# Optimization experiments

Hardware: AMD Instinct MI355X
Metric: run time of the kernel (lower is better)

Reference implementation:

```python
import jax, jax.numpy as jnp
import numpy as np

B, L, D = 4, 4096, 1024


def hippo_freqs(dim):
    n = np.arange(dim, dtype=np.float32)
    f = np.sqrt(2 * n + 1)
    f = f / f.max()
    return np.exp(-f * np.log(10000)).astype(np.float32)


def setup_inputs() -> dict:
    key = jax.random.key(0)
    ks = jax.random.split(key, 8)
    s = 1.0 / np.sqrt(D)
    return {
        "x": jax.random.normal(ks[0], (B, L, D), dtype=jnp.float32),
        "omega": jnp.asarray(hippo_freqs(D)),
        "log_gamma": jax.random.normal(ks[1], (D,), dtype=jnp.float32) - 3.0,
        "dt": jnp.float32(0.1),
        "W_psi": jax.random.uniform(ks[2], (2 * D, D), jnp.float32, -s, s),
        "b_psi": jax.random.uniform(ks[3], (2 * D,), jnp.float32, -s, s),
        "W_phi": jax.random.uniform(ks[4], (2 * D, D), jnp.float32, -s, s),
        "b_phi": jax.random.uniform(ks[5], (2 * D,), jnp.float32, -s, s),
        "W_gate": jax.random.uniform(ks[6], (D, D), jnp.float32, -s, s),
        "b_gate": jax.random.uniform(ks[7], (D,), jnp.float32, -s, s),
    }


def _proj(z):
    # exact_projection: per-channel-axis standardization over last dim (biased var)
    mean = z.mean(axis=-1, keepdims=True)
    var = ((z - mean) ** 2).mean(axis=-1, keepdims=True)
    return (z - mean) / (jnp.sqrt(var) + 1e-6)


def reference(x, omega, log_gamma, dt, W_psi, b_psi, W_phi, b_phi, W_gate, b_gate):
    Bn, Ln, Dn = x.shape
    psi_raw = jnp.einsum("bld,ed->ble", x, W_psi) + b_psi
    phi_raw = jnp.einsum("bld,ed->ble", x, W_phi) + b_phi
    psi = jax.lax.complex(psi_raw[..., :Dn], psi_raw[..., Dn:])
    phi = jax.lax.complex(phi_raw[..., :Dn], phi_raw[..., Dn:])
    gate = jax.nn.sigmoid(jnp.einsum("bld,ed->ble", x, W_gate) + b_gate)
    U = gate.astype(psi.dtype) * psi  # [B,L,D] complex

    dt_abs = jnp.abs(dt)
    lam = jax.lax.complex(-jnp.exp(log_gamma), omega)  # [D]
    t_axis = jnp.arange(Ln, dtype=jnp.float32)
    kernel = jnp.exp(lam[None, :] * t_axis[:, None].astype(lam.dtype) * dt_abs)  # [L,D]

    n_fft = 2 * Ln
    Kf = jnp.fft.fft(kernel, n=n_fft, axis=0)          # [2L,D]
    Uf = jnp.fft.fft(U, n=n_fft, axis=1)               # [B,2L,D]
    H = jnp.fft.ifft(Uf * Kf[None], axis=1)[:, :Ln]    # causal conv, [B,L,D]

    H_proj = jax.lax.complex(_proj(H.real), _proj(H.imag))
    return (H_proj * jnp.conj(phi)).real
```

## Files before the change

kernel.cpp:

```cpp
#include <hip/hip_runtime.h>
#include <hip/hip_bf16.h>
#include <math.h>

#define B_ 4
#define L_ 4096
#define D_ 1024
#define M_ (B_*L_)
#define N_ 5120
#define K_ 1024
#define CHUNKS 128
#define LC 32
#define PL ((long)M_ * D_)

#define WS_NEEDED 211812352ull

typedef __attribute__((ext_vector_type(8))) short bf16x8;
typedef __attribute__((ext_vector_type(4))) float f32x4;

__global__ void convert_kernel(const float* __restrict__ x,
                               const float* __restrict__ Wpsi,
                               const float* __restrict__ Wphi,
                               const float* __restrict__ Wgate,
                               __hip_bfloat16* __restrict__ xb,
                               __hip_bfloat16* __restrict__ wb) {
    long i0 = (long)blockIdx.x * blockDim.x + threadIdx.x;
    long stride = (long)gridDim.x * blockDim.x;
    const long nx = (long)M_ * K_;
    for (long j = i0; j < nx; j += stride) xb[j] = __float2bfloat16(x[j]);
    const long nW1 = 2048L * 1024, nW2 = 2048L * 1024, nW3 = 1024L * 1024;
    for (long j = i0; j < nW1; j += stride) wb[j] = __float2bfloat16(Wpsi[j]);
    for (long j = i0; j < nW2; j += stride) wb[nW1 + j] = __float2bfloat16(Wphi[j]);
    for (long j = i0; j < nW3; j += stride) wb[nW1 + nW2 + j] = __float2bfloat16(Wgate[j]);
}

#define BM 128
#define BN 128
#define BK 64
__global__ __launch_bounds__(256) void gemm_kernel(const __hip_bfloat16* __restrict__ xb,
                                                   const __hip_bfloat16* __restrict__ wb,
                                                   const float* __restrict__ b_psi,
                                                   const float* __restrict__ b_phi,
                                                   const float* __restrict__ b_gate,
                                                   __hip_bfloat16* __restrict__ raw5) {
    __shared__ __hip_bfloat16 As[BM * BK];
    __shared__ __hip_bfloat16 Bs[BN * BK];

    const int tid  = threadIdx.x;
    const int wave = tid >> 6;
    const int lane = tid & 63;
    const int row16 = lane & 15;
    const int quad  = lane >> 4;
    const int m_blk = blockIdx.x * BM;
    const int n_blk = blockIdx.y * BN;
    const int m_off = (wave >> 1) * 64;
    const int n_off = (wave & 1) * 64;

    const int sub_r = lane >> 3;
    const int ci    = lane & 7;

    f32x4 acc[4][4] = {};

    for (int k0 = 0; k0 < K_; k0 += BK) {
        __syncthreads();
#pragma unroll
        for (int j2 = 0; j2 < 4; j2++) {
            int j  = wave * 4 + j2;
            int r  = j * 8 + sub_r;
            int gc = ci ^ (r & 7);
            const __hip_bfloat16* ga = xb + (long)(m_blk + r) * K_ + k0 + gc * 8;
            const __hip_bfloat16* gb = wb + (long)(n_blk + r) * K_ + k0 + gc * 8;
            __builtin_amdgcn_global_load_lds(
                (const __attribute__((address_space(1))) void*)ga,
                (__attribute__((address_space(3))) void*)((char*)As + j * 1024),
                16, 0, 0);
            __builtin_amdgcn_global_load_lds(
                (const __attribute__((address_space(1))) void*)gb,
                (__attribute__((address_space(3))) void*)((char*)Bs + j * 1024),
                16, 0, 0);
        }
        __syncthreads();

#pragma unroll
        for (int ks = 0; ks < 2; ks++) {
            bf16x8 a[4], b[4];
            int c = ks * 4 + quad;
#pragma unroll
            for (int t = 0; t < 4; t++) {
                int ra = m_off + t * 16 + row16;
                a[t] = *(const bf16x8*)((const char*)As + ra * 128 + ((c ^ (ra & 7)) * 16));
                int rb = n_off + t * 16 + row16;
                b[t] = *(const bf16x8*)((const char*)Bs + rb * 128 + ((c ^ (rb & 7)) * 16));
            }
#pragma unroll
            for (int mi = 0; mi < 4; mi++)
#pragma unroll
                for (int ni = 0; ni < 4; ni++)
                    acc[mi][ni] = __builtin_amdgcn_mfma_f32_16x16x32_bf16(a[mi], b[ni], acc[mi][ni], 0, 0, 0);
        }
    }

#pragma unroll
    for (int mi = 0; mi < 4; mi++) {
#pragma unroll
        for (int ni = 0; ni < 4; ni++) {
            int n = n_blk + n_off + ni * 16 + row16;
            float bias = (n < 2048) ? b_psi[n] : (n < 4096) ? b_phi[n - 2048] : b_gate[n - 4096];
            int g = n >> 10, d = n & 1023;
            __hip_bfloat16* pl = raw5 + (long)g * PL;
#pragma unroll
            for (int r = 0; r < 4; r++) {
                int m = m_blk + m_off + mi * 16 + quad * 4 + r;
                pl[(long)m * D_ + d] = __float2bfloat16(acc[mi][ni][r] + bias);
            }
        }
    }
}

__global__ __launch_bounds__(1024) void scan1_kernel(const __hip_bfloat16* __restrict__ raw5,
                                                     const float* __restrict__ omega,
                                                     const float* __restrict__ log_gamma,
                                                     const float* __restrict__ dtp,
                                                     float2* __restrict__ E) {
    const int d = threadIdx.x;
    const int c = blockIdx.x;
    const int b = blockIdx.y;
    const float dt = fabsf(dtp[0]);
    const float decay = expf(-expf(log_gamma[d]) * dt);
    const float ang = omega[d] * dt;
    const float ar = decay * cosf(ang), ai = decay * sinf(ang);

    const __hip_bfloat16* Pre = raw5;
    const __hip_bfloat16* Pim = raw5 + PL;
    const __hip_bfloat16* Gt  = raw5 + 4 * PL;
    long base = (long)(b * L_ + c * LC) * D_ + d;

    float hr = 0.f, hi = 0.f;
    for (int i = 0; i < LC; i++) {
        long idx = base + (long)i * D_;
        float sg = 1.f / (1.f + expf(-__bfloat162float(Gt[idx])));
        float ur = sg * __bfloat162float(Pre[idx]);
        float ui = sg * __bfloat162float(Pim[idx]);
        float nhr = ar * hr - ai * hi + ur;
        float nhi = ar * hi + ai * hr + ui;
        hr = nhr; hi = nhi;
    }
    E[((long)c * B_ + b) * D_ + d] = make_float2(hr, hi);
}

__global__ void carry_kernel(const float2* __restrict__ E,
                             const float* __restrict__ omega,
                             const float* __restrict__ log_gamma,
                             const float* __restrict__ dtp,
                             float2* __restrict__ carry) {
    int t = blockIdx.x * blockDim.x + threadIdx.x;
    int b = t >> 10, d = t & 1023;
    const float dt = fabsf(dtp[0]);
    const float decay = expf(-expf(log_gamma[d]) * dt * (float)LC);
    const float ang = omega[d] * dt * (float)LC;
    const float Ar = decay * cosf(ang), Ai = decay * sinf(ang);
    float sr = 0.f, si = 0.f;
    for (int c = 0; c < CHUNKS; c++) {
        long idx = ((long)c * B_ + b) * D_ + d;
        carry[idx] = make_float2(sr, si);
        float2 e = E[idx];
        float nr = e.x + Ar * sr - Ai * si;
        float ni = e.y + Ar * si + Ai * sr;
        sr = nr; si = ni;
    }
}

__global__ __launch_bounds__(1024) void scan2_kernel(const __hip_bfloat16* __restrict__ raw5,
                                                     const float2* __restrict__ carry,
                                                     const float* __restrict__ omega,
                                                     const float* __restrict__ log_gamma,
                                                     const float* __restrict__ dtp,
                                                     float* __restrict__ out) {
    const int d = threadIdx.x;
    const int c = blockIdx.x;
    const int b = blockIdx.y;
    const float dt = fabsf(dtp[0]);
    const float decay = expf(-expf(log_gamma[d]) * dt);
    const float ang = omega[d] * dt;
    const float ar = decay * cosf(ang), ai = decay * sinf(ang);

    float2 h0 = carry[((long)c * B_ + b) * D_ + d];
    float hr = h0.x, hi = h0.y;

    __shared__ float red[16][4];
    __shared__ float stats[4];
    const int lane = threadIdx.x & 63, wv = threadIdx.x >> 6;

    const __hip_bfloat16* Ure = raw5;
    const __hip_bfloat16* Uim = raw5 + PL;
    const __hip_bfloat16* Pre = raw5 + 2 * PL;
    const __hip_bfloat16* Pim = raw5 + 3 * PL;
    const __hip_bfloat16* Gt  = raw5 + 4 * PL;
    long base = (long)(b * L_ + c * LC) * D_ + d;

    for (int i = 0; i < LC; i++) {
        long idx = base + (long)i * D_;
        float sg = 1.f / (1.f + expf(-__bfloat162float(Gt[idx])));
        float ur = sg * __bfloat162float(Ure[idx]);
        float ui = sg * __bfloat162float(Uim[idx]);
        float nhr = ar * hr - ai * hi + ur;
        float nhi = ar * hi + ai * hr + ui;
        hr = nhr; hi = nhi;

        float s0 = hr, s1 = hr * hr, s2 = hi, s3 = hi * hi;
        for (int off = 32; off; off >>= 1) {
            s0 += __shfl_down(s0, off);
            s1 += __shfl_down(s1, off);
            s2 += __shfl_down(s2, off);
            s3 += __shfl_down(s3, off);
        }
        if (lane == 0) { red[wv][0] = s0; red[wv][1] = s1; red[wv][2] = s2; red[wv][3] = s3; }
        __syncthreads();
        if (wv == 0 && lane < 4) {
            float t = 0.f;
#pragma unroll
            for (int w = 0; w < 16; w++) t += red[w][lane];
            stats[lane] = t;
        }
        __syncthreads();
        float mean_r = stats[0] * (1.f / D_);
        float var_r  = stats[1] * (1.f / D_) - mean_r * mean_r;
        float mean_i = stats[2] * (1.f / D_);
        float var_i  = stats[3] * (1.f / D_) - mean_i * mean_i;
        float inv_r = 1.f / (sqrtf(fmaxf(var_r, 0.f)) + 1e-6f);
        float inv_i = 1.f / (sqrtf(fmaxf(var_i, 0.f)) + 1e-6f);
        float pr = __bfloat162float(Pre[idx]);
        float pi = __bfloat162float(Pim[idx]);
        out[idx] = (hr - mean_r) * inv_r * pr + (hi - mean_i) * inv_i * pi;
    }
}

extern "C" void kernel_launch(void* const* d_in, const int* in_sizes, int n_in,
                              void* d_out, int out_size, void* d_ws, size_t ws_size,
                              hipStream_t stream) {
    (void)in_sizes; (void)n_in; (void)out_size;
    if (ws_size < WS_NEEDED) return;

    const float* x         = (const float*)d_in[0];
    const float* omega     = (const float*)d_in[1];
    const float* log_gamma = (const float*)d_in[2];
    const float* dt        = (const float*)d_in[3];
    const float* W_psi     = (const float*)d_in[4];
    const float* b_psi     = (const float*)d_in[5];
    const float* W_phi     = (const float*)d_in[6];
    const float* b_phi     = (const float*)d_in[7];
    const float* W_gate    = (const float*)d_in[8];
    const float* b_gate    = (const float*)d_in[9];

    char* ws = (char*)d_ws;
    __hip_bfloat16* xb   = (__hip_bfloat16*)(ws);
    __hip_bfloat16* wb   = (__hip_bfloat16*)(ws + 33554432);
    __hip_bfloat16* raw5 = (__hip_bfloat16*)(ws + 44040192);
    float2* E     = (float2*)(ws);
    float2* carry = (float2*)(ws + 4194304);
    float* out = (float*)d_out;

    convert_kernel<<<2048, 256, 0, stream>>>(x, W_psi, W_phi, W_gate, xb, wb);
    gemm_kernel<<<dim3(M_ / BM, N_ / BN), 256, 0, stream>>>(xb, wb, b_psi, b_phi, b_gate, raw5);
    scan1_kernel<<<dim3(CHUNKS, B_), 1024, 0, stream>>>(raw5, omega, log_gamma, dt, E);
    carry_kernel<<<16, 256, 0, stream>>>(E, omega, log_gamma, dt, carry);
    scan2_kernel<<<dim3(CHUNKS, B_), 1024, 0, stream>>>(raw5, carry, omega, log_gamma, dt, out);
}
```

Before: 510.2 us.

## Store local scan states, parallelize carry scan, and fuse normalization into a finish pass

The first scan pass now writes each local chunk state back in place over the psi planes. The carry propagation becomes a parallel Hillis-Steele scan with one block per (batch, channel). A new finish kernel reconstructs the full state as local state plus precomputed A^(i+1) times carry, and computes per-row mean and variance with one wave per row using vectorized loads and no block barriers. The conversion kernel is also vectorized to float4 reads. This removes the serial per-step reduction and the two __syncthreads per timestep from the old second scan, at the cost of storing intermediate states in bf16 and adding an apow table.

Result: faster. 485.0 us (-4.9%).

```diff
diff --git a/kernel.cpp b/kernel.cpp
--- a/kernel.cpp
+++ b/kernel.cpp
@@ -17,20 +17,33 @@
 typedef __attribute__((ext_vector_type(8))) short bf16x8;
 typedef __attribute__((ext_vector_type(4))) float f32x4;
 
+__device__ inline float b2f(short s) {
+    unsigned u = ((unsigned)(unsigned short)s) << 16;
+    float f; __builtin_memcpy(&f, &u, 4); return f;
+}
+
+__device__ inline void cvt4(const float4* __restrict__ src, ushort* __restrict__ dst, long j) {
+    float4 v = src[j];
+    __hip_bfloat16 a = __float2bfloat16(v.x), b = __float2bfloat16(v.y),
+                   c = __float2bfloat16(v.z), d = __float2bfloat16(v.w);
+    ushort4 o = { *(ushort*)&a, *(ushort*)&b, *(ushort*)&c, *(ushort*)&d };
+    *(ushort4*)(dst + j * 4) = o;
+}
+
 __global__ void convert_kernel(const float* __restrict__ x,
                                const float* __restrict__ Wpsi,
                                const float* __restrict__ Wphi,
                                const float* __restrict__ Wgate,
-                               __hip_bfloat16* __restrict__ xb,
-                               __hip_bfloat16* __restrict__ wb) {
+                               ushort* __restrict__ xb,
+                               ushort* __restrict__ wb) {
     long i0 = (long)blockIdx.x * blockDim.x + threadIdx.x;
     long stride = (long)gridDim.x * blockDim.x;
-    const long nx = (long)M_ * K_;
-    for (long j = i0; j < nx; j += stride) xb[j] = __float2bfloat16(x[j]);
-    const long nW1 = 2048L * 1024, nW2 = 2048L * 1024, nW3 = 1024L * 1024;
-    for (long j = i0; j < nW1; j += stride) wb[j] = __float2bfloat16(Wpsi[j]);
-    for (long j = i0; j < nW2; j += stride) wb[nW1 + j] = __float2bfloat16(Wphi[j]);
-    for (long j = i0; j < nW3; j += stride) wb[nW1 + nW2 + j] = __float2bfloat16(Wgate[j]);
+    const long nx4 = ((long)M_ * K_) >> 2;
+    for (long j = i0; j < nx4; j += stride) cvt4((const float4*)x, xb, j);
+    const long nW14 = (2048L * 1024) >> 2, nW34 = (1024L * 1024) >> 2;
+    for (long j = i0; j < nW14; j += stride) cvt4((const float4*)Wpsi, wb, j);
+    for (long j = i0; j < nW14; j += stride) cvt4((const float4*)Wphi, wb + 2048L * 1024, j);
+    for (long j = i0; j < nW34; j += stride) cvt4((const float4*)Wgate, wb + 4096L * 1024, j);
 }
 
 #define BM 128
@@ -116,7 +129,7 @@
     }
 }
 
-__global__ __launch_bounds__(1024) void scan1_kernel(const __hip_bfloat16* __restrict__ raw5,
+__global__ __launch_bounds__(1024) void scan1_kernel(__hip_bfloat16* raw5,
                                                      const float* __restrict__ omega,
                                                      const float* __restrict__ log_gamma,
                                                      const float* __restrict__ dtp,
@@ -129,9 +142,9 @@
     const float ang = omega[d] * dt;
     const float ar = decay * cosf(ang), ai = decay * sinf(ang);
 
-    const __hip_bfloat16* Pre = raw5;
-    const __hip_bfloat16* Pim = raw5 + PL;
-    const __hip_bfloat16* Gt  = raw5 + 4 * PL;
+    __hip_bfloat16* Pre = raw5;
+    __hip_bfloat16* Pim = raw5 + PL;
+    const __hip_bfloat16* Gt = raw5 + 4 * PL;
     long base = (long)(b * L_ + c * LC) * D_ + d;
 
     float hr = 0.f, hi = 0.f;
@@ -143,95 +156,123 @@
         float nhr = ar * hr - ai * hi + ur;
         float nhi = ar * hi + ai * hr + ui;
         hr = nhr; hi = nhi;
+        Pre[idx] = __float2bfloat16(hr);
+        Pim[idx] = __float2bfloat16(hi);
     }
     E[((long)c * B_ + b) * D_ + d] = make_float2(hr, hi);
 }
 
-__global__ void carry_kernel(const float2* __restrict__ E,
-                             const float* __restrict__ omega,
-                             const float* __restrict__ log_gamma,
-                             const float* __restrict__ dtp,
-                             float2* __restrict__ carry) {
+__global__ void apow_kernel(const float* __restrict__ omega,
+                            const float* __restrict__ log_gamma,
+                            const float* __restrict__ dtp,
+                            float2* __restrict__ apow) {
     int t = blockIdx.x * blockDim.x + threadIdx.x;
-    int b = t >> 10, d = t & 1023;
+    int i = t >> 10, d = t & 1023;
+    float dt = fabsf(dtp[0]);
+    float e = expf(-expf(log_gamma[d]) * dt * (float)(i + 1));
+    float ang = omega[d] * dt * (float)(i + 1);
+    apow[t] = make_float2(e * cosf(ang), e * sinf(ang));
+}
+
+__global__ __launch_bounds__(128) void carry_kernel(const float2* __restrict__ E,
+                                                    const float* __restrict__ omega,
+                                                    const float* __restrict__ log_gamma,
+                                                    const float* __restrict__ dtp,
+                                                    float2* __restrict__ carry) {
+    __shared__ float2 sh[CHUNKS];
+    const int c = threadIdx.x;
+    const int bd = blockIdx.x;
+    const int b = bd >> 10, d = bd & 1023;
     const float dt = fabsf(dtp[0]);
-    const float decay = expf(-expf(log_gamma[d]) * dt * (float)LC);
-    const float ang = omega[d] * dt * (float)LC;
-    const float Ar = decay * cosf(ang), Ai = decay * sinf(ang);
-    float sr = 0.f, si = 0.f;
-    for (int c = 0; c < CHUNKS; c++) {
-        long idx = ((long)c * B_ + b) * D_ + d;
-        carry[idx] = make_float2(sr, si);
-        float2 e = E[idx];
-        float nr = e.x + Ar * sr - Ai * si;
-        float ni = e.y + Ar * si + Ai * sr;
-        sr = nr; si = ni;
-    }
-}
-
-__global__ __launch_bounds__(1024) void scan2_kernel(const __hip_bfloat16* __restrict__ raw5,
+    const float gd = expf(log_gamma[d]);
+    const float wd = omega[d];
+
+    float2 v = E[((long)c * B_ + b) * D_ + d];
+    sh[c] = v;
+    __syncthreads();
+#pragma unroll
+    for (int s = 1; s < CHUNKS; s <<= 1) {
+        float2 prev;
+        bool has = (c >= s);
+        if (has) prev = sh[c - s];
+        __syncthreads();
+        if (has) {
+            float t = dt * (float)LC * (float)s;
+            float dec = expf(-gd * t);
+            float ang = wd * t;
+            float Ar = dec * cosf(ang), Ai = dec * sinf(ang);
+            v.x += Ar * prev.x - Ai * prev.y;
+            v.y += Ar * prev.y + Ai * prev.x;
+            sh[c] = v;
+        }
+        __syncthreads();
+    }
+    float2 outv = (c == 0) ? make_float2(0.f, 0.f) : sh[c - 1];
+    carry[((long)c * B_ + b) * D_ + d] = outv;
+}
+
+__global__ __launch_bounds__(256) void finish_kernel(const __hip_bfloat16* __restrict__ raw5,
                                                      const float2* __restrict__ carry,
-                                                     const float* __restrict__ omega,
-                                                     const float* __restrict__ log_gamma,
-                                                     const float* __restrict__ dtp,
+                                                     const float2* __restrict__ apow,
                                                      float* __restrict__ out) {
-    const int d = threadIdx.x;
-    const int c = blockIdx.x;
-    const int b = blockIdx.y;
-    const float dt = fabsf(dtp[0]);
-    const float decay = expf(-expf(log_gamma[d]) * dt);
-    const float ang = omega[d] * dt;
-    const float ar = decay * cosf(ang), ai = decay * sinf(ang);
-
-    float2 h0 = carry[((long)c * B_ + b) * D_ + d];
-    float hr = h0.x, hi = h0.y;
-
-    __shared__ float red[16][4];
-    __shared__ float stats[4];
-    const int lane = threadIdx.x & 63, wv = threadIdx.x >> 6;
-
-    const __hip_bfloat16* Ure = raw5;
-    const __hip_bfloat16* Uim = raw5 + PL;
+    const int wv = threadIdx.x >> 6, lane = threadIdx.x & 63;
+    const int r = blockIdx.x * 4 + wv;
+    const int l = r & (L_ - 1);
+    const int b = r >> 12;
+    const int c = l >> 5, i = l & 31;
+    const int d0 = lane * 16;
+    const long base = (long)r * D_ + d0;
+
+    const __hip_bfloat16* Hre = raw5;
+    const __hip_bfloat16* Him = raw5 + PL;
     const __hip_bfloat16* Pre = raw5 + 2 * PL;
     const __hip_bfloat16* Pim = raw5 + 3 * PL;
-    const __hip_bfloat16* Gt  = raw5 + 4 * PL;
-    long base = (long)(b * L_ + c * LC) * D_ + d;
-
-    for (int i = 0; i < LC; i++) {
-        long idx = base + (long)i * D_;
-        float sg = 1.f / (1.f + expf(-__bfloat162float(Gt[idx])));
-        float ur = sg * __bfloat162float(Ure[idx]);
-        float ui = sg * __bfloat162float(Uim[idx]);
-        float nhr = ar * hr - ai * hi + ur;
-        float nhi = ar * hi + ai * hr + ui;
-        hr = nhr; hi = nhi;
-
-        float s0 = hr, s1 = hr * hr, s2 = hi, s3 = hi * hi;
-        for (int off = 32; off; off >>= 1) {
-            s0 += __shfl_down(s0, off);
-            s1 += __shfl_down(s1, off);
-            s2 += __shfl_down(s2, off);
-            s3 += __shfl_down(s3, off);
-        }
-        if (lane == 0) { red[wv][0] = s0; red[wv][1] = s1; red[wv][2] = s2; red[wv][3] = s3; }
-        __syncthreads();
-        if (wv == 0 && lane < 4) {
-            float t = 0.f;
-#pragma unroll
-            for (int w = 0; w < 16; w++) t += red[w][lane];
-            stats[lane] = t;
-        }
-        __syncthreads();
-        float mean_r = stats[0] * (1.f / D_);
-        float var_r  = stats[1] * (1.f / D_) - mean_r * mean_r;
-        float mean_i = stats[2] * (1.f / D_);
-        float var_i  = stats[3] * (1.f / D_) - mean_i * mean_i;
-        float inv_r = 1.f / (sqrtf(fmaxf(var_r, 0.f)) + 1e-6f);
-        float inv_i = 1.f / (sqrtf(fmaxf(var_i, 0.f)) + 1e-6f);
-        float pr = __bfloat162float(Pre[idx]);
-        float pi = __bfloat162float(Pim[idx]);
-        out[idx] = (hr - mean_r) * inv_r * pr + (hi - mean_i) * inv_i * pi;
-    }
+    const float2* cr = carry + ((long)c * B_ + b) * D_ + d0;
+    const float2* ap = apow + (long)i * D_ + d0;
+
+    bf16x8 hre[2], him[2];
+    hre[0] = *(const bf16x8*)(Hre + base);     hre[1] = *(const bf16x8*)(Hre + base + 8);
+    him[0] = *(const bf16x8*)(Him + base);     him[1] = *(const bf16x8*)(Him + base + 8);
+
+    float hr[16], hi[16];
+    float s0 = 0.f, s1 = 0.f, s2 = 0.f, s3 = 0.f;
+#pragma unroll
+    for (int j = 0; j < 16; j++) {
+        float2 cv = cr[j];
+        float2 av = ap[j];
+        float fr = av.x * cv.x - av.y * cv.y;
+        float fi = av.x * cv.y + av.y * cv.x;
+        float xr = b2f(hre[j >> 3][j & 7]) + fr;
+        float xi = b2f(him[j >> 3][j & 7]) + fi;
+        hr[j] = xr; hi[j] = xi;
+        s0 += xr; s1 += xr * xr; s2 += xi; s3 += xi * xi;
+    }
+#pragma unroll
+    for (int m = 1; m < 64; m <<= 1) {
+        s0 += __shfl_xor(s0, m);
+        s1 += __shfl_xor(s1, m);
+        s2 += __shfl_xor(s2, m);
+        s3 += __shfl_xor(s3, m);
+    }
+    float mean_r = s0 * (1.f / D_);
+    float var_r  = s1 * (1.f / D_) - mean_r * mean_r;
+    float mean_i = s2 * (1.f / D_);
+    float var_i  = s3 * (1.f / D_) - mean_i * mean_i;
+    float inv_r = 1.f / (sqrtf(fmaxf(var_r, 0.f)) + 1e-6f);
+    float inv_i = 1.f / (sqrtf(fmaxf(var_i, 0.f)) + 1e-6f);
+
+    bf16x8 pre[2], pim[2];
+    pre[0] = *(const bf16x8*)(Pre + base);     pre[1] = *(const bf16x8*)(Pre + base + 8);
+    pim[0] = *(const bf16x8*)(Pim + base);     pim[1] = *(const bf16x8*)(Pim + base + 8);
+
+    float o[16];
+#pragma unroll
+    for (int j = 0; j < 16; j++)
+        o[j] = (hr[j] - mean_r) * inv_r * b2f(pre[j >> 3][j & 7])
+             + (hi[j] - mean_i) * inv_i * b2f(pim[j >> 3][j & 7]);
+#pragma unroll
+    for (int q = 0; q < 4; q++)
+        *(float4*)(out + base + q * 4) = make_float4(o[q*4], o[q*4+1], o[q*4+2], o[q*4+3]);
 }
 
 extern "C" void kernel_launch(void* const* d_in, const int* in_sizes, int n_in,
@@ -257,11 +298,13 @@
     __hip_bfloat16* raw5 = (__hip_bfloat16*)(ws + 44040192);
     float2* E     = (float2*)(ws);
     float2* carry = (float2*)(ws + 4194304);
+    float2* apow  = (float2*)(ws + 8388608);
     float* out = (float*)d_out;
 
-    convert_kernel<<<2048, 256, 0, stream>>>(x, W_psi, W_phi, W_gate, xb, wb);
+    convert_kernel<<<2048, 256, 0, stream>>>(x, W_psi, W_phi, W_gate, (ushort*)xb, (ushort*)wb);
     gemm_kernel<<<dim3(M_ / BM, N_ / BN), 256, 0, stream>>>(xb, wb, b_psi, b_phi, b_gate, raw5);
+    apow_kernel<<<128, 256, 0, stream>>>(omega, log_gamma, dt, apow);
     scan1_kernel<<<dim3(CHUNKS, B_), 1024, 0, stream>>>(raw5, omega, log_gamma, dt, E);
-    carry_kernel<<<16, 256, 0, stream>>>(E, omega, log_gamma, dt, carry);
-    scan2_kernel<<<dim3(CHUNKS, B_), 1024, 0, stream>>>(raw5, carry, omega, log_gamma, dt, out);
-}
+    carry_kernel<<<B_ * D_, 128, 0, stream>>>(E, omega, log_gamma, dt, carry);
+    finish_kernel<<<M_ / 4, 256, 0, stream>>>(raw5, carry, apow, out);
+}
```
